# Performance work log

Hardware: AMD Instinct MI355X
Metric: run time of the kernel (lower is better)

## Reference

```python
import jax, jax.numpy as jnp
import numpy as np

B, N, C = 4, 2048, 768
H = 12
D = C // H  # head_dim = 64
SCALE = D ** -0.5


def setup_inputs() -> dict:
    key = jax.random.key(0)
    ks = jax.random.split(key, 9)
    x_q = jax.random.normal(ks[0], (B, N, C), dtype=jnp.float32)
    x_k = jax.random.normal(ks[1], (B, N, C), dtype=jnp.float32)
    x_v = jax.random.normal(ks[2], (B, N, C), dtype=jnp.float32)
    x_u = jax.random.uniform(ks[3], (B, N, C), dtype=jnp.float32)
    s = C ** -0.5
    Wq = jax.random.normal(ks[4], (C, C), dtype=jnp.float32) * s
    Wk = jax.random.normal(ks[5], (C, C), dtype=jnp.float32) * s
    Wv = jax.random.normal(ks[6], (C, C), dtype=jnp.float32) * s
    Wp = jax.random.normal(ks[7], (C, C), dtype=jnp.float32) * s
    bp = jax.random.normal(ks[8], (C,), dtype=jnp.float32) * 0.01
    return {"x_q": x_q, "x_k": x_k, "x_v": x_v, "x_u": x_u,
            "Wq": Wq, "Wk": Wk, "Wv": Wv, "Wp": Wp, "bp": bp}


def reference(x_q, x_k, x_v, x_u, Wq, Wk, Wv, Wp, bp):
    # Linear projections (torch Linear: y = x @ W.T), split into heads [B,H,N,D]
    def to_heads(x, W):
        y = jnp.einsum('bnc,oc->bno', x, W)
        return y.reshape(B, N, H, D).transpose(0, 2, 1, 3)
    q = to_heads(x_q, Wq) * SCALE
    k = to_heads(x_k, Wk)
    v = to_heads(x_v, Wv)
    # Scores [B,H,N,N]
    attn = jnp.einsum('bhqd,bhkd->bhqk', q, k)
    # Uncertainty map: per-query scalar (mean over channels), broadcast over keys & heads
    uc = jnp.mean(x_u, axis=-1)  # [B,N]
    attn = attn * uc[:, None, :, None]
    attn = jax.nn.softmax(attn, axis=-1)
    out = jnp.einsum('bhqk,bhkd->bhqd', attn, v)
    out = out.transpose(0, 2, 1, 3).reshape(B, N, C)
    return jnp.einsum('bnc,oc->bno', out, Wp) + bp
```

## Files before the change

kernel.cpp:

```cpp
#include <hip/hip_runtime.h>
#include <hip/hip_bf16.h>
#include <cstdint>

#define B_ 4
#define N_ 2048
#define C_ 768
#define H_ 12
#define D_ 64
#define QSCALE 0.18033688011112042f

typedef __bf16 bf16x8 __attribute__((ext_vector_type(8)));
typedef float f32x4 __attribute__((ext_vector_type(4)));

__device__ __forceinline__ unsigned f2bs(float x) {
  unsigned u = __builtin_bit_cast(unsigned, x);
  unsigned r = (u + 0x7fffu + ((u >> 16) & 1u)) >> 16;
  return r;
}

__device__ __forceinline__ bf16x8 ldb8(const unsigned short* p) {
  return __builtin_bit_cast(bf16x8, *(const uint4*)p);
}

__device__ __forceinline__ f32x4 mfma16(bf16x8 a, bf16x8 b, f32x4 c) {
  return __builtin_amdgcn_mfma_f32_16x16x32_bf16(a, b, c, 0, 0, 0);
}

__device__ __forceinline__ void async16(const unsigned short* g, unsigned short* l) {
  __builtin_amdgcn_global_load_lds(
      (const __attribute__((address_space(1))) unsigned int*)g,
      (__attribute__((address_space(3))) unsigned int*)l, 16, 0, 0);
}

__global__ void convx_kernel(const float* __restrict__ s0, const float* __restrict__ s1,
                             const float* __restrict__ s2,
                             unsigned short* __restrict__ d0, unsigned short* __restrict__ d1,
                             unsigned short* __restrict__ d2) {
  const float* s; unsigned short* d;
  switch (blockIdx.y) {
    case 0: s = s0; d = d0; break;
    case 1: s = s1; d = d1; break;
    default: s = s2; d = d2; break;
  }
  int i = (blockIdx.x * 256 + threadIdx.x) * 4;
  float4 v = *(const float4*)(s + i);
  ushort4 h;
  h.x = (unsigned short)f2bs(v.x); h.y = (unsigned short)f2bs(v.y);
  h.z = (unsigned short)f2bs(v.z); h.w = (unsigned short)f2bs(v.w);
  *(ushort4*)(d + i) = h;
}

__global__ void convw_kernel(const float* __restrict__ s0, const float* __restrict__ s1,
                             const float* __restrict__ s2, const float* __restrict__ s3,
                             unsigned short* __restrict__ d0, unsigned short* __restrict__ d1,
                             unsigned short* __restrict__ d2, unsigned short* __restrict__ d3) {
  const float* s; unsigned short* d;
  switch (blockIdx.y) {
    case 0: s = s0; d = d0; break;
    case 1: s = s1; d = d1; break;
    case 2: s = s2; d = d2; break;
    default: s = s3; d = d3; break;
  }
  int i = (blockIdx.x * 256 + threadIdx.x) * 4;
  float4 v = *(const float4*)(s + i);
  ushort4 h;
  h.x = (unsigned short)f2bs(v.x); h.y = (unsigned short)f2bs(v.y);
  h.z = (unsigned short)f2bs(v.z); h.w = (unsigned short)f2bs(v.w);
  *(ushort4*)(d + i) = h;
}

__global__ void uc_kernel(const float* __restrict__ xu, float* __restrict__ uc) {
  int w = threadIdx.x >> 6, lane = threadIdx.x & 63;
  int row = blockIdx.x * 4 + w;
  const float* p = xu + (size_t)row * C_;
  float s = 0.f;
#pragma unroll
  for (int i = 0; i < 3; ++i) {
    float4 v = *(const float4*)(p + (i * 64 + lane) * 4);
    s += v.x + v.y + v.z + v.w;
  }
#pragma unroll
  for (int off = 1; off < 64; off <<= 1) s += __shfl_xor(s, off);
  if (lane == 0) uc[row] = s * (1.f / 768.f);
}

__device__ __forceinline__ void gemm_mainloop(
    const unsigned short* __restrict__ A, const unsigned short* __restrict__ W,
    int m0, int n0, unsigned short* Al, unsigned short* Bl,
    int tid, int wm, int wn, int quad, int id15, f32x4 (*acc)[4]) {
  const int wb = tid & 192;
  const unsigned short* ap[4];
  const unsigned short* bp[4];
#pragma unroll
  for (int s = 0; s < 4; ++s) {
    int g = s * 256 + tid;
    int row = (g >> 2) & 127;
    int col = ((g >> 9) << 5) | ((g & 3) << 3);
    ap[s] = A + (size_t)(m0 + row) * C_ + col;
    bp[s] = W + (size_t)(n0 + row) * C_ + col;
  }

  for (int kt = 0; kt < C_; kt += 64) {
    __syncthreads();
#pragma unroll
    for (int s = 0; s < 4; ++s) {
      async16(ap[s] + kt, Al + (s * 256 + wb) * 8);
      async16(bp[s] + kt, Bl + (s * 256 + wb) * 8);
    }
    __syncthreads();

#pragma unroll
    for (int kk = 0; kk < 2; ++kk) {
      bf16x8 af[4], bfr[4];
#pragma unroll
      for (int i = 0; i < 4; ++i)
        af[i]  = ldb8(&Al[kk * 4096 + (wm + i * 16 + id15) * 32 + quad * 8]);
#pragma unroll
      for (int j = 0; j < 4; ++j)
        bfr[j] = ldb8(&Bl[kk * 4096 + (wn + j * 16 + id15) * 32 + quad * 8]);
#pragma unroll
      for (int i = 0; i < 4; ++i)
#pragma unroll
        for (int j = 0; j < 4; ++j)
          acc[i][j] = mfma16(af[i], bfr[j], acc[i][j]);
    }
  }
}

#define TSTR 136
__global__ __launch_bounds__(256, 3) void gemm_qkv(
    const unsigned short* __restrict__ xq, const unsigned short* __restrict__ xk,
    const unsigned short* __restrict__ xv,
    const unsigned short* __restrict__ wq, const unsigned short* __restrict__ wk,
    const unsigned short* __restrict__ wv,
    unsigned short* __restrict__ oq, unsigned short* __restrict__ ok,
    unsigned short* __restrict__ ov, const float* __restrict__ uc) {
  __shared__ __align__(16) unsigned short S[128 * TSTR];
  unsigned short* Al = S;
  unsigned short* Bl = S + 8192;
  const int tid = threadIdx.x;
  const int w = tid >> 6, lane = tid & 63, quad = lane >> 4, id15 = lane & 15;
  const int wm = (w >> 1) << 6, wn = (w & 1) << 6;
  const int m0 = blockIdx.y << 7, n0 = blockIdx.x << 7;
  const int z = blockIdx.z;

  const unsigned short* A = (z == 0) ? xq : (z == 1) ? xk : xv;
  const unsigned short* W = (z == 0) ? wq : (z == 1) ? wk : wv;

  f32x4 acc[4][4] = {};
  gemm_mainloop(A, W, m0, n0, Al, Bl, tid, wm, wn, quad, id15, acc);

  if (z == 2) {
    __syncthreads();
#pragma unroll
    for (int i = 0; i < 4; ++i)
#pragma unroll
      for (int j = 0; j < 4; ++j) {
        uint2 u;
        u.x = f2bs(acc[i][j][0]) | (f2bs(acc[i][j][1]) << 16);
        u.y = f2bs(acc[i][j][2]) | (f2bs(acc[i][j][3]) << 16);
        *(uint2*)&S[(wn + j * 16 + id15) * TSTR + wm + i * 16 + quad * 4] = u;
      }
    __syncthreads();
    const int b = m0 >> 11, nb = m0 & (N_ - 1);
#pragma unroll
    for (int s = 0; s < 8; ++s) {
      int c = s * 256 + tid;
      int row = c >> 4, o = (c & 15) << 3;
      *(uint4*)(ov + (size_t)(b * C_ + n0 + row) * N_ + nb + o) = *(const uint4*)&S[row * TSTR + o];
    }
    return;
  }

#pragma unroll
  for (int i = 0; i < 4; ++i) {
#pragma unroll
    for (int j = 0; j < 4; ++j) {
#pragma unroll
      for (int r = 0; r < 4; ++r) {
        int gm = m0 + wm + i * 16 + quad * 4 + r;
        int gn = n0 + wn + j * 16 + id15;
        float v = acc[i][j][r];
        if (z == 0) {
          v *= QSCALE * uc[gm];
          oq[(size_t)gm * C_ + gn] = (unsigned short)f2bs(v);
        } else {
          ok[(size_t)gm * C_ + gn] = (unsigned short)f2bs(v);
        }
      }
    }
  }
}

__global__ __launch_bounds__(256, 3) void gemm_out(
    const unsigned short* __restrict__ ao, const unsigned short* __restrict__ wp,
    float* __restrict__ out, const float* __restrict__ bias) {
  __shared__ __align__(16) unsigned short Al[128 * 64];
  __shared__ __align__(16) unsigned short Bl[128 * 64];
  const int tid = threadIdx.x;
  const int w = tid >> 6, lane = tid & 63, quad = lane >> 4, id15 = lane & 15;
  const int wm = (w >> 1) << 6, wn = (w & 1) << 6;
  const int m0 = blockIdx.y << 7, n0 = blockIdx.x << 7;

  f32x4 acc[4][4] = {};
  gemm_mainloop(ao, wp, m0, n0, Al, Bl, tid, wm, wn, quad, id15, acc);

#pragma unroll
  for (int i = 0; i < 4; ++i) {
#pragma unroll
    for (int j = 0; j < 4; ++j) {
#pragma unroll
      for (int r = 0; r < 4; ++r) {
        int gm = m0 + wm + i * 16 + quad * 4 + r;
        int gn = n0 + wn + j * 16 + id15;
        out[(size_t)gm * C_ + gn] = acc[i][j][r] + bias[gn];
      }
    }
  }
}

#define KSTR 72
#define PSTR 72
__global__ __launch_bounds__(256, 3) void attn_kernel(
    const unsigned short* __restrict__ Q, const unsigned short* __restrict__ Kk,
    const unsigned short* __restrict__ Vt, unsigned short* __restrict__ O) {
  __shared__ __align__(16) unsigned short Kl[64 * KSTR];
  __shared__ __align__(16) unsigned short Vl[64 * KSTR];
  __shared__ __align__(16) unsigned short Pl[8][16 * PSTR];

  const int tid = threadIdx.x;
  const int w = tid >> 6, lane = tid & 63, quad = lane >> 4, id15 = lane & 15;
  const int bh = blockIdx.y;
  const int b = bh / H_, h = bh % H_;
  const int q0 = blockIdx.x * 128 + w * 32;

  bf16x8 qf[2][2];
#pragma unroll
  for (int rg = 0; rg < 2; ++rg)
#pragma unroll
    for (int kb = 0; kb < 2; ++kb)
      qf[rg][kb] = ldb8(Q + (size_t)(b * N_ + q0 + rg * 16 + id15) * C_ + h * 64 + kb * 32 + quad * 8);

  const uint4 onesu = {0x3F803F80u, 0x3F803F80u, 0x3F803F80u, 0x3F803F80u};
  const bf16x8 onesf = __builtin_bit_cast(bf16x8, onesu);

  f32x4 oacc[2][4] = {};
  f32x4 lacc[2] = {};

  const size_t kbase = (size_t)(b * N_) * C_ + h * 64;
  const size_t vbase = (size_t)(b * C_ + h * 64) * N_;
  const int srow0 = tid >> 3, srow1 = (256 + tid) >> 3;
  const int sseg0 = (tid & 7) << 3;

  unsigned short* Plw0 = &Pl[w * 2 + 0][0];
  unsigned short* Plw1 = &Pl[w * 2 + 1][0];

  for (int kc = 0; kc < N_; kc += 64) {
    __syncthreads();
    *(uint4*)&Kl[srow0 * KSTR + sseg0] = *(const uint4*)(Kk + kbase + (size_t)(kc + srow0) * C_ + sseg0);
    *(uint4*)&Kl[srow1 * KSTR + sseg0] = *(const uint4*)(Kk + kbase + (size_t)(kc + srow1) * C_ + sseg0);
    *(uint4*)&Vl[srow0 * KSTR + sseg0] = *(const uint4*)(Vt + vbase + (size_t)srow0 * N_ + kc + sseg0);
    *(uint4*)&Vl[srow1 * KSTR + sseg0] = *(const uint4*)(Vt + vbase + (size_t)srow1 * N_ + kc + sseg0);
    __syncthreads();

    f32x4 sA[4], sB[4];
#pragma unroll
    for (int cb = 0; cb < 4; ++cb) {
      f32x4 a = {}, c = {};
#pragma unroll
      for (int kb = 0; kb < 2; ++kb) {
        bf16x8 kf = ldb8(&Kl[(cb * 16 + id15) * KSTR + kb * 32 + quad * 8]);
        a = mfma16(kf, qf[0][kb], a);
        c = mfma16(kf, qf[1][kb], c);
      }
      sA[cb] = a; sB[cb] = c;
    }

#pragma unroll
    for (int rg = 0; rg < 2; ++rg) {
      f32x4* s4 = (rg == 0) ? sA : sB;
      unsigned short* Plw = (rg == 0) ? Plw0 : Plw1;
#pragma unroll
      for (int cb = 0; cb < 4; ++cb) {
        unsigned p0 = __builtin_bit_cast(unsigned, exp2f(s4[cb][0]));
        unsigned p1 = __builtin_bit_cast(unsigned, exp2f(s4[cb][1]));
        unsigned p2 = __builtin_bit_cast(unsigned, exp2f(s4[cb][2]));
        unsigned p3 = __builtin_bit_cast(unsigned, exp2f(s4[cb][3]));
        uint2 u;
        u.x = __builtin_amdgcn_perm(p1, p0, 0x07060302u);
        u.y = __builtin_amdgcn_perm(p3, p2, 0x07060302u);
        *(uint2*)&Plw[id15 * PSTR + cb * 16 + quad * 4] = u;
      }
    }

    bf16x8 pf[2][2];
#pragma unroll
    for (int kb = 0; kb < 2; ++kb) {
      pf[0][kb] = ldb8(&Plw0[id15 * PSTR + kb * 32 + quad * 8]);
      pf[1][kb] = ldb8(&Plw1[id15 * PSTR + kb * 32 + quad * 8]);
    }

#pragma unroll
    for (int kb = 0; kb < 2; ++kb) {
      lacc[0] = mfma16(pf[0][kb], onesf, lacc[0]);
      lacc[1] = mfma16(pf[1][kb], onesf, lacc[1]);
    }
#pragma unroll
    for (int db = 0; db < 4; ++db) {
#pragma unroll
      for (int kb = 0; kb < 2; ++kb) {
        bf16x8 vf = ldb8(&Vl[(db * 16 + id15) * KSTR + kb * 32 + quad * 8]);
        oacc[0][db] = mfma16(pf[0][kb], vf, oacc[0][db]);
        oacc[1][db] = mfma16(pf[1][kb], vf, oacc[1][db]);
      }
    }
  }

#pragma unroll
  for (int rg = 0; rg < 2; ++rg) {
#pragma unroll
    for (int r = 0; r < 4; ++r) {
      float linv = 1.0f / lacc[rg][r];
      int n = q0 + rg * 16 + quad * 4 + r;
#pragma unroll
      for (int db = 0; db < 4; ++db)
        O[(size_t)(b * N_ + n) * C_ + h * 64 + db * 16 + id15] = (unsigned short)f2bs(oacc[rg][db][r] * linv);
    }
  }
}

extern "C" void kernel_launch(void* const* d_in, const int* in_sizes, int n_in,
                              void* d_out, int out_size, void* d_ws, size_t ws_size,
                              hipStream_t stream) {
  const float* x_q = (const float*)d_in[0];
  const float* x_k = (const float*)d_in[1];
  const float* x_v = (const float*)d_in[2];
  const float* x_u = (const float*)d_in[3];
  const float* Wq  = (const float*)d_in[4];
  const float* Wk  = (const float*)d_in[5];
  const float* Wv  = (const float*)d_in[6];
  const float* Wp  = (const float*)d_in[7];
  const float* bp  = (const float*)d_in[8];

  char* ws = (char*)d_ws;
  size_t off = 0;
  auto alloc = [&](size_t bytes) {
    char* p = ws + off;
    off += (bytes + 255) & ~(size_t)255;
    return p;
  };
  unsigned short* wq16 = (unsigned short*)alloc((size_t)C_ * C_ * 2);
  unsigned short* wk16 = (unsigned short*)alloc((size_t)C_ * C_ * 2);
  unsigned short* wv16 = (unsigned short*)alloc((size_t)C_ * C_ * 2);
  unsigned short* wp16 = (unsigned short*)alloc((size_t)C_ * C_ * 2);
  float*          ucp  = (float*)alloc((size_t)B_ * N_ * 4);
  unsigned short* xq16 = (unsigned short*)alloc((size_t)B_ * N_ * C_ * 2);
  unsigned short* xk16 = (unsigned short*)alloc((size_t)B_ * N_ * C_ * 2);
  unsigned short* xv16 = (unsigned short*)alloc((size_t)B_ * N_ * C_ * 2);
  unsigned short* q_s  = (unsigned short*)alloc((size_t)B_ * N_ * C_ * 2);
  unsigned short* k_s  = (unsigned short*)alloc((size_t)B_ * N_ * C_ * 2);
  unsigned short* vT   = (unsigned short*)alloc((size_t)B_ * N_ * C_ * 2);
  unsigned short* ao   = (unsigned short*)alloc((size_t)B_ * N_ * C_ * 2);

  convx_kernel<<<dim3(6144, 3), 256, 0, stream>>>(x_q, x_k, x_v, xq16, xk16, xv16);
  convw_kernel<<<dim3(576, 4), 256, 0, stream>>>(Wq, Wk, Wv, Wp, wq16, wk16, wv16, wp16);
  uc_kernel<<<dim3(2048), 256, 0, stream>>>(x_u, ucp);
  gemm_qkv<<<dim3(6, 64, 3), 256, 0, stream>>>(xq16, xk16, xv16, wq16, wk16, wv16,
                                               q_s, k_s, vT, ucp);
  attn_kernel<<<dim3(16, 48), 256, 0, stream>>>(q_s, k_s, vT, ao);
  gemm_out<<<dim3(6, 64), 256, 0, stream>>>(ao, wp16, (float*)d_out, bp);
}
```

Before: 313.5 us.

## Fuse prep kernels, add XCD-aware block swizzle, shrink out-GEMM tile to 64x128

Merges the three conversion/mean kernels into one launch to cut launch overhead. Remaps block indices in the QKV GEMM, attention and output GEMM so that blocks sharing the same head or row band land on the same XCD, which should improve L2 reuse across the chiplets. The output projection now uses 64x128 tiles with its own main loop and allows 4 blocks per CU, doubling the block count from 384 to 768 to better fill the 256 CUs. The smaller tiles mean less reuse of each loaded tile, and the hand-coded index mapping relies on the exact grid sizes.

Result: faster. 296.4 us (-5.4%).

```diff
diff --git a/kernel.cpp b/kernel.cpp
--- a/kernel.cpp
+++ b/kernel.cpp
@@ -32,56 +32,52 @@
       (__attribute__((address_space(3))) unsigned int*)l, 16, 0, 0);
 }
 
-__global__ void convx_kernel(const float* __restrict__ s0, const float* __restrict__ s1,
-                             const float* __restrict__ s2,
-                             unsigned short* __restrict__ d0, unsigned short* __restrict__ d1,
-                             unsigned short* __restrict__ d2) {
-  const float* s; unsigned short* d;
-  switch (blockIdx.y) {
-    case 0: s = s0; d = d0; break;
-    case 1: s = s1; d = d1; break;
-    default: s = s2; d = d2; break;
-  }
-  int i = (blockIdx.x * 256 + threadIdx.x) * 4;
-  float4 v = *(const float4*)(s + i);
-  ushort4 h;
-  h.x = (unsigned short)f2bs(v.x); h.y = (unsigned short)f2bs(v.y);
-  h.z = (unsigned short)f2bs(v.z); h.w = (unsigned short)f2bs(v.w);
-  *(ushort4*)(d + i) = h;
-}
-
-__global__ void convw_kernel(const float* __restrict__ s0, const float* __restrict__ s1,
-                             const float* __restrict__ s2, const float* __restrict__ s3,
-                             unsigned short* __restrict__ d0, unsigned short* __restrict__ d1,
-                             unsigned short* __restrict__ d2, unsigned short* __restrict__ d3) {
-  const float* s; unsigned short* d;
-  switch (blockIdx.y) {
-    case 0: s = s0; d = d0; break;
-    case 1: s = s1; d = d1; break;
-    case 2: s = s2; d = d2; break;
-    default: s = s3; d = d3; break;
-  }
-  int i = (blockIdx.x * 256 + threadIdx.x) * 4;
-  float4 v = *(const float4*)(s + i);
-  ushort4 h;
-  h.x = (unsigned short)f2bs(v.x); h.y = (unsigned short)f2bs(v.y);
-  h.z = (unsigned short)f2bs(v.z); h.w = (unsigned short)f2bs(v.w);
-  *(ushort4*)(d + i) = h;
-}
-
-__global__ void uc_kernel(const float* __restrict__ xu, float* __restrict__ uc) {
-  int w = threadIdx.x >> 6, lane = threadIdx.x & 63;
-  int row = blockIdx.x * 4 + w;
-  const float* p = xu + (size_t)row * C_;
-  float s = 0.f;
-#pragma unroll
-  for (int i = 0; i < 3; ++i) {
-    float4 v = *(const float4*)(p + (i * 64 + lane) * 4);
-    s += v.x + v.y + v.z + v.w;
-  }
-#pragma unroll
-  for (int off = 1; off < 64; off <<= 1) s += __shfl_xor(s, off);
-  if (lane == 0) uc[row] = s * (1.f / 768.f);
+__global__ void prep_kernel(
+    const float* __restrict__ xq, const float* __restrict__ xk,
+    const float* __restrict__ xv, const float* __restrict__ xu,
+    const float* __restrict__ Wq, const float* __restrict__ Wk,
+    const float* __restrict__ Wv, const float* __restrict__ Wp,
+    unsigned short* __restrict__ dxq, unsigned short* __restrict__ dxk,
+    unsigned short* __restrict__ dxv,
+    unsigned short* __restrict__ dwq, unsigned short* __restrict__ dwk,
+    unsigned short* __restrict__ dwv, unsigned short* __restrict__ dwp,
+    float* __restrict__ uc) {
+  const int id = blockIdx.x;
+  if (id < 18432) {
+    const float* s = (id < 6144) ? xq : (id < 12288) ? xk : xv;
+    unsigned short* d = (id < 6144) ? dxq : (id < 12288) ? dxk : dxv;
+    int i = ((id % 6144) * 256 + threadIdx.x) * 4;
+    float4 v = *(const float4*)(s + i);
+    ushort4 h;
+    h.x = (unsigned short)f2bs(v.x); h.y = (unsigned short)f2bs(v.y);
+    h.z = (unsigned short)f2bs(v.z); h.w = (unsigned short)f2bs(v.w);
+    *(ushort4*)(d + i) = h;
+  } else if (id < 20736) {
+    int sub = id - 18432;
+    int which = sub / 576;
+    const float* s = (which == 0) ? Wq : (which == 1) ? Wk : (which == 2) ? Wv : Wp;
+    unsigned short* d = (which == 0) ? dwq : (which == 1) ? dwk : (which == 2) ? dwv : dwp;
+    int i = ((sub % 576) * 256 + threadIdx.x) * 4;
+    float4 v = *(const float4*)(s + i);
+    ushort4 h;
+    h.x = (unsigned short)f2bs(v.x); h.y = (unsigned short)f2bs(v.y);
+    h.z = (unsigned short)f2bs(v.z); h.w = (unsigned short)f2bs(v.w);
+    *(ushort4*)(d + i) = h;
+  } else {
+    int sub = id - 20736;
+    int w = threadIdx.x >> 6, lane = threadIdx.x & 63;
+    int row = sub * 4 + w;
+    const float* p = xu + (size_t)row * C_;
+    float s = 0.f;
+#pragma unroll
+    for (int i = 0; i < 3; ++i) {
+      float4 v = *(const float4*)(p + (i * 64 + lane) * 4);
+      s += v.x + v.y + v.z + v.w;
+    }
+#pragma unroll
+    for (int off = 1; off < 64; off <<= 1) s += __shfl_xor(s, off);
+    if (lane == 0) uc[row] = s * (1.f / 768.f);
+  }
 }
 
 __device__ __forceinline__ void gemm_mainloop(
@@ -141,8 +137,11 @@
   const int tid = threadIdx.x;
   const int w = tid >> 6, lane = tid & 63, quad = lane >> 4, id15 = lane & 15;
   const int wm = (w >> 1) << 6, wn = (w & 1) << 6;
-  const int m0 = blockIdx.y << 7, n0 = blockIdx.x << 7;
-  const int z = blockIdx.z;
+  const int id = blockIdx.x;
+  const int xcd = id & 7, slot = id >> 3;
+  const int n0 = (slot % 6) << 7;
+  const int gz = xcd * 24 + slot / 6;
+  const int z = gz >> 6, m0 = (gz & 63) << 7;
 
   const unsigned short* A = (z == 0) ? xq : (z == 1) ? xk : xv;
   const unsigned short* W = (z == 0) ? wq : (z == 1) ? wk : wv;
@@ -192,21 +191,65 @@
   }
 }
 
-__global__ __launch_bounds__(256, 3) void gemm_out(
+__global__ __launch_bounds__(256, 4) void gemm_out(
     const unsigned short* __restrict__ ao, const unsigned short* __restrict__ wp,
     float* __restrict__ out, const float* __restrict__ bias) {
-  __shared__ __align__(16) unsigned short Al[128 * 64];
+  __shared__ __align__(16) unsigned short Al[64 * 64];
   __shared__ __align__(16) unsigned short Bl[128 * 64];
   const int tid = threadIdx.x;
   const int w = tid >> 6, lane = tid & 63, quad = lane >> 4, id15 = lane & 15;
-  const int wm = (w >> 1) << 6, wn = (w & 1) << 6;
-  const int m0 = blockIdx.y << 7, n0 = blockIdx.x << 7;
-
-  f32x4 acc[4][4] = {};
-  gemm_mainloop(ao, wp, m0, n0, Al, Bl, tid, wm, wn, quad, id15, acc);
-
-#pragma unroll
-  for (int i = 0; i < 4; ++i) {
+  const int wm = (w >> 1) << 5, wn = (w & 1) << 6;
+  const int id = blockIdx.x;
+  const int xcd = id & 7, slot = id >> 3;
+  const int n0 = (slot % 6) << 7;
+  const int m0 = (xcd * 16 + slot / 6) << 6;
+
+  const int wb = tid & 192;
+  const unsigned short* ap[2];
+#pragma unroll
+  for (int s = 0; s < 2; ++s) {
+    int g = s * 256 + tid;
+    int row = (g >> 2) & 63;
+    int col = ((g >> 8) << 5) | ((g & 3) << 3);
+    ap[s] = ao + (size_t)(m0 + row) * C_ + col;
+  }
+  const unsigned short* bp[4];
+#pragma unroll
+  for (int s = 0; s < 4; ++s) {
+    int g = s * 256 + tid;
+    int row = (g >> 2) & 127;
+    int col = ((g >> 9) << 5) | ((g & 3) << 3);
+    bp[s] = wp + (size_t)(n0 + row) * C_ + col;
+  }
+
+  f32x4 acc[2][4] = {};
+  for (int kt = 0; kt < C_; kt += 64) {
+    __syncthreads();
+#pragma unroll
+    for (int s = 0; s < 2; ++s) async16(ap[s] + kt, Al + (s * 256 + wb) * 8);
+#pragma unroll
+    for (int s = 0; s < 4; ++s) async16(bp[s] + kt, Bl + (s * 256 + wb) * 8);
+    __syncthreads();
+
+#pragma unroll
+    for (int kk = 0; kk < 2; ++kk) {
+      bf16x8 af[2], bfr[4];
+#pragma unroll
+      for (int i = 0; i < 2; ++i)
+        af[i]  = ldb8(&Al[kk * 2048 + (wm + i * 16 + id15) * 32 + quad * 8]);
+#pragma unroll
+      for (int j = 0; j < 4; ++j)
+        bfr[j] = ldb8(&Bl[kk * 4096 + (wn + j * 16 + id15) * 32 + quad * 8]);
+#pragma unroll
+      for (int i = 0; i < 2; ++i)
+#pragma unroll
+        for (int j = 0; j < 4; ++j)
+          acc[i][j] = mfma16(af[i], bfr[j], acc[i][j]);
+    }
+  }
+
+#pragma unroll
+  for (int i = 0; i < 2; ++i) {
 #pragma unroll
     for (int j = 0; j < 4; ++j) {
 #pragma unroll
@@ -230,9 +273,12 @@
 
   const int tid = threadIdx.x;
   const int w = tid >> 6, lane = tid & 63, quad = lane >> 4, id15 = lane & 15;
-  const int bh = blockIdx.y;
+  const int id = blockIdx.x;
+  const int xcd = id & 7, slot = id >> 3;
+  const int bh = xcd * 6 + (slot >> 4);
+  const int qt = slot & 15;
   const int b = bh / H_, h = bh % H_;
-  const int q0 = blockIdx.x * 128 + w * 32;
+  const int q0 = qt * 128 + w * 32;
 
   bf16x8 qf[2][2];
 #pragma unroll
@@ -362,11 +408,11 @@
   unsigned short* vT   = (unsigned short*)alloc((size_t)B_ * N_ * C_ * 2);
   unsigned short* ao   = (unsigned short*)alloc((size_t)B_ * N_ * C_ * 2);
 
-  convx_kernel<<<dim3(6144, 3), 256, 0, stream>>>(x_q, x_k, x_v, xq16, xk16, xv16);
-  convw_kernel<<<dim3(576, 4), 256, 0, stream>>>(Wq, Wk, Wv, Wp, wq16, wk16, wv16, wp16);
-  uc_kernel<<<dim3(2048), 256, 0, stream>>>(x_u, ucp);
-  gemm_qkv<<<dim3(6, 64, 3), 256, 0, stream>>>(xq16, xk16, xv16, wq16, wk16, wv16,
-                                               q_s, k_s, vT, ucp);
-  attn_kernel<<<dim3(16, 48), 256, 0, stream>>>(q_s, k_s, vT, ao);
-  gemm_out<<<dim3(6, 64), 256, 0, stream>>>(ao, wp16, (float*)d_out, bp);
-}
+  prep_kernel<<<dim3(22784), 256, 0, stream>>>(x_q, x_k, x_v, x_u, Wq, Wk, Wv, Wp,
+                                               xq16, xk16, xv16,
+                                               wq16, wk16, wv16, wp16, ucp);
+  gemm_qkv<<<dim3(1152), 256, 0, stream>>>(xq16, xk16, xv16, wq16, wk16, wv16,
+                                           q_s, k_s, vT, ucp);
+  attn_kernel<<<dim3(768), 256, 0, stream>>>(q_s, k_s, vT, ao);
+  gemm_out<<<dim3(768), 256, 0, stream>>>(ao, wp16, (float*)d_out, bp);
+}
```
